# Performance work log

Measured on AMD Instinct MI355X. Metric: run time of the kernel, lower is better.

The kernel has to match this reference:

```python
import jax, jax.numpy as jnp
import numpy as np


def setup_inputs() -> dict:
    key = jax.random.key(0)
    k1, k2, k3, k4 = jax.random.split(key, 4)
    B, S, D, R = 32, 512, 1024, 256
    batch = jax.random.normal(k1, (B, S, D), dtype=jnp.float32)
    # params initialized uniform(-0.05, 0.05) in the original
    proj_L = jax.random.uniform(k2, (D, R), minval=-0.05, maxval=0.05, dtype=jnp.float32)
    proj_R = jax.random.uniform(k3, (R, D), minval=-0.05, maxval=0.05, dtype=jnp.float32)
    bias = jax.random.uniform(k4, (1,), minval=-0.05, maxval=0.05, dtype=jnp.float32)
    return {"batch": batch, "proj_L": proj_L, "proj_R": proj_R, "bias": bias}


def reference(batch, proj_L, proj_R, bias):
    # logits[b,i,j] = batch[b,i] @ (L @ R) @ batch[b,j] + bias
    # Computed as (batch @ L) @ (batch @ R^T)^T -- two batched GEMMs,
    # avoiding the O(B*S^2*D) expanded intermediate of the original.
    # Dropout is identity in eval mode.
    left = jnp.einsum('bsd,dr->bsr', batch, proj_L)   # [B,S,R]
    right = jnp.einsum('rd,btd->brt', proj_R, batch)  # [B,R,S]
    logits = jnp.einsum('bsr,brt->bst', left, right) + bias[0]
    return logits
```

## Files before the change

kernel.cpp:

```cpp
#include <hip/hip_runtime.h>
#include <hip/hip_bf16.h>
#include <stdint.h>

typedef __attribute__((ext_vector_type(8))) __bf16 bf16x8;
typedef __attribute__((ext_vector_type(4))) float f32x4;

static constexpr int Bb = 32, Ss = 512, Dd = 1024, Rr = 256;

__device__ __forceinline__ void gload_lds16(const void* g, void* l) {
  __builtin_amdgcn_global_load_lds(
      (const __attribute__((address_space(1))) void*)g,
      (__attribute__((address_space(3))) void*)l, 16, 0, 0);
}

__global__ __launch_bounds__(256) void prep_kernel(
    const float* __restrict__ L, const float* __restrict__ R,
    __bf16* __restrict__ Bt) {
  int i = blockIdx.x * 256 + threadIdx.x;
  int n = i >> 10;
  int d = i & (Dd - 1);
  float v = (n < Rr) ? L[d * Rr + n] : R[(size_t)(n - Rr) * Dd + d];
  Bt[i] = (__bf16)v;
}

__global__ __launch_bounds__(512, 2) void proj_gemm(
    const float* __restrict__ batch,
    const __bf16* __restrict__ Bt,
    __bf16* __restrict__ outL,
    __bf16* __restrict__ outR) {
  const int s = (blockIdx.x & 7) * 32 + (blockIdx.x >> 3);
  const int mt = s >> 1;
  const int nt = s & 1;
  const int m0 = mt * 128, n0 = nt * 256;

  __shared__ __align__(16) char smem[49152];

  const int t = threadIdx.x;
  const int lane = t & 63;
  const int wave = t >> 6;
  const int wr = wave >> 2, wc = wave & 3;

  f32x4 acc[4][4] = {};
  f32x4 areg0, areg1;

  const int arow = t >> 2, ag = t & 3;
  const int ags = ag ^ ((arow >> 1) & 3);

  auto issueA = [&](int k0) {
    const float* src = batch + (size_t)(m0 + arow) * Dd + k0 + ag * 8;
    areg0 = *(const f32x4*)src;
    areg1 = *(const f32x4*)(src + 4);
  };
  auto writeA = [&](int buf) {
    bf16x8 v;
    v[0] = (__bf16)areg0[0]; v[1] = (__bf16)areg0[1];
    v[2] = (__bf16)areg0[2]; v[3] = (__bf16)areg0[3];
    v[4] = (__bf16)areg1[0]; v[5] = (__bf16)areg1[1];
    v[6] = (__bf16)areg1[2]; v[7] = (__bf16)areg1[3];
    *(bf16x8*)(smem + buf * 8192 + (arow * 4 + ags) * 16) = v;
  };
  auto stageB = [&](int buf, int k0) {
#pragma unroll
    for (int p = 0; p < 2; ++p) {
      int e = p * 512 + t;
      int row = e >> 2, g = e & 3;
      int gs = g ^ ((row >> 1) & 3);
      gload_lds16(Bt + (size_t)(n0 + row) * Dd + k0 + gs * 8,
                  smem + 16384 + buf * 16384 + e * 16);
    }
  };
  auto compute = [&](int buf) {
    const char* Ab = smem + buf * 8192;
    const char* Bb = smem + 16384 + buf * 16384;
    bf16x8 a[4], b[4];
    const int g = lane >> 4;
#pragma unroll
    for (int m = 0; m < 4; ++m) {
      int row = wr * 64 + m * 16 + (lane & 15);
      a[m] = *(const bf16x8*)(Ab + (row * 4 + (g ^ ((row >> 1) & 3))) * 16);
    }
#pragma unroll
    for (int n = 0; n < 4; ++n) {
      int row = wc * 64 + n * 16 + (lane & 15);
      b[n] = *(const bf16x8*)(Bb + (row * 4 + (g ^ ((row >> 1) & 3))) * 16);
    }
#pragma unroll
    for (int m = 0; m < 4; ++m)
#pragma unroll
      for (int n = 0; n < 4; ++n)
        acc[m][n] = __builtin_amdgcn_mfma_f32_16x16x32_bf16(a[m], b[n],
                                                            acc[m][n], 0, 0, 0);
  };

  issueA(0);
  stageB(0, 0);
  writeA(0);
  int cur = 0;
  for (int it = 0; it < 32; ++it) {
    if (it < 31) {
      issueA(it * 32 + 32);
      stageB(cur ^ 1, it * 32 + 32);
      asm volatile("s_waitcnt vmcnt(4)" ::: "memory");
    } else {
      asm volatile("s_waitcnt vmcnt(0)" ::: "memory");
    }
    __builtin_amdgcn_s_barrier();
    compute(cur);
    if (it < 31) writeA(cur ^ 1);
    asm volatile("s_waitcnt lgkmcnt(0)" ::: "memory");
    __builtin_amdgcn_s_barrier();
    cur ^= 1;
  }

  __bf16* out = nt ? outR : outL;
  const int col = lane & 15, rgrp = lane >> 4;
#pragma unroll
  for (int m = 0; m < 4; ++m) {
    int r0 = m0 + wr * 64 + m * 16 + rgrp * 4;
#pragma unroll
    for (int n = 0; n < 4; ++n) {
      int c = wc * 64 + n * 16 + col;
#pragma unroll
      for (int i = 0; i < 4; ++i)
        out[(size_t)(r0 + i) * Rr + c] = (__bf16)acc[m][n][i];
    }
  }
}

__global__ __launch_bounds__(256, 4) void score_gemm(
    const __bf16* __restrict__ left,
    const __bf16* __restrict__ right,
    const float* __restrict__ biasp,
    float* __restrict__ out) {
  const int nt = blockIdx.x;
  const int mt = blockIdx.y;
  const int bz = blockIdx.z;
  const __bf16* A = left + (size_t)bz * Ss * Rr;
  const __bf16* B = right + (size_t)bz * Ss * Rr;
  float* O = out + (size_t)bz * Ss * Ss;
  const int m0 = mt * 64, n0 = nt * 128;

  __shared__ __align__(16) char smem[24576];

  const int t = threadIdx.x;
  const int lane = t & 63;
  const int wave = t >> 6;
  const int wr = wave >> 1, wc = wave & 1;

  f32x4 acc[2][4] = {};

  for (int it = 0; it < 4; ++it) {
    const int k0 = it * 64;
    __syncthreads();
#pragma unroll
    for (int q = 0; q < 2; ++q) {
      int e = q * 256 + t;
      int row = e >> 3, g = e & 7;
      int gsrc = g ^ (row & 7);
      gload_lds16(A + (size_t)(m0 + row) * Rr + k0 + gsrc * 8, smem + e * 16);
    }
#pragma unroll
    for (int q = 0; q < 4; ++q) {
      int e = q * 256 + t;
      int row = e >> 3, g = e & 7;
      int gsrc = g ^ (row & 7);
      gload_lds16(B + (size_t)(n0 + row) * Rr + k0 + gsrc * 8,
                  smem + 8192 + e * 16);
    }
    __syncthreads();

#pragma unroll
    for (int kk = 0; kk < 2; ++kk) {
      bf16x8 a[2], b[4];
#pragma unroll
      for (int m = 0; m < 2; ++m) {
        int row = wr * 32 + m * 16 + (lane & 15);
        int g = kk * 4 + (lane >> 4);
        a[m] = *(const bf16x8*)(smem + (row * 8 + (g ^ (row & 7))) * 16);
      }
#pragma unroll
      for (int n = 0; n < 4; ++n) {
        int row = wc * 64 + n * 16 + (lane & 15);
        int g = kk * 4 + (lane >> 4);
        b[n] = *(const bf16x8*)(smem + 8192 +
                                (row * 8 + (g ^ (row & 7))) * 16);
      }
#pragma unroll
      for (int m = 0; m < 2; ++m)
#pragma unroll
        for (int n = 0; n < 4; ++n)
          acc[m][n] = __builtin_amdgcn_mfma_f32_16x16x32_bf16(a[m], b[n],
                                                              acc[m][n], 0, 0, 0);
    }
  }

  const float bias = *biasp;
  const int col = lane & 15, rgrp = lane >> 4;
#pragma unroll
  for (int m = 0; m < 2; ++m) {
    int r0 = m0 + wr * 32 + m * 16 + rgrp * 4;
#pragma unroll
    for (int n = 0; n < 4; ++n) {
      int c = n0 + wc * 64 + n * 16 + col;
#pragma unroll
      for (int i = 0; i < 4; ++i)
        O[(size_t)(r0 + i) * Ss + c] = acc[m][n][i] + bias;
    }
  }
}

extern "C" void kernel_launch(void* const* d_in, const int* in_sizes, int n_in,
                              void* d_out, int out_size, void* d_ws,
                              size_t ws_size, hipStream_t stream) {
  const float* batch = (const float*)d_in[0];
  const float* projL = (const float*)d_in[1];
  const float* projR = (const float*)d_in[2];
  const float* bias = (const float*)d_in[3];
  float* out = (float*)d_out;

  char* ws = (char*)d_ws;
  __bf16* left = (__bf16*)(ws);
  __bf16* right = (__bf16*)(ws + 8388608);
  __bf16* Btc = (__bf16*)(ws + 16777216);

  prep_kernel<<<dim3(2048), dim3(256), 0, stream>>>(projL, projR, Btc);
  proj_gemm<<<dim3(256), dim3(512), 0, stream>>>(batch, Btc, left, right);
  score_gemm<<<dim3(4, 8, 32), dim3(256), 0, stream>>>(left, right, bias, out);
}
```

Baseline: 54.28 us.

## Reshape projection GEMM tile to 256x128 with K=64 stages

The projection GEMM tile changes from 128x256 to 256x128, and each pipeline step now covers 64 elements of K instead of 32. That halves the number of barrier-separated iterations. The LDS layout moves to an 8-group XOR swizzle, and the loop is restructured: the next A and B tiles are issued before compute, and the wait and barrier come after the LDS write. The cost is a larger LDS footprint (96KB), which likely limits residency to one block per CU. Each batch row is also now read by four N-tiles instead of two, so the kernel leans more on L2 reuse.

```diff
diff --git a/kernel.cpp b/kernel.cpp
--- a/kernel.cpp
+++ b/kernel.cpp
@@ -28,98 +28,115 @@
     const __bf16* __restrict__ Bt,
     __bf16* __restrict__ outL,
     __bf16* __restrict__ outR) {
-  const int s = (blockIdx.x & 7) * 32 + (blockIdx.x >> 3);
-  const int mt = s >> 1;
-  const int nt = s & 1;
-  const int m0 = mt * 128, n0 = nt * 256;
-
-  __shared__ __align__(16) char smem[49152];
+  const int s = ((blockIdx.x & 7) << 5) + (blockIdx.x >> 3);
+  const int mt = s >> 2;
+  const int nt = s & 3;
+  const int m0 = mt * 256, n0 = nt * 128;
+
+  __shared__ __align__(16) char smem[98304];
 
   const int t = threadIdx.x;
   const int lane = t & 63;
   const int wave = t >> 6;
-  const int wr = wave >> 2, wc = wave & 3;
+  const int wr = wave >> 1, wc = wave & 1;
 
   f32x4 acc[4][4] = {};
-  f32x4 areg0, areg1;
-
-  const int arow = t >> 2, ag = t & 3;
-  const int ags = ag ^ ((arow >> 1) & 3);
+  f32x4 areg[8];
 
   auto issueA = [&](int k0) {
-    const float* src = batch + (size_t)(m0 + arow) * Dd + k0 + ag * 8;
-    areg0 = *(const f32x4*)src;
-    areg1 = *(const f32x4*)(src + 4);
+#pragma unroll
+    for (int q = 0; q < 4; ++q) {
+      int e = q * 512 + t;
+      int row = e >> 3, g = e & 7;
+      const float* src = batch + (size_t)(m0 + row) * Dd + k0 + g * 8;
+      areg[2 * q] = *(const f32x4*)src;
+      areg[2 * q + 1] = *(const f32x4*)(src + 4);
+    }
   };
   auto writeA = [&](int buf) {
-    bf16x8 v;
-    v[0] = (__bf16)areg0[0]; v[1] = (__bf16)areg0[1];
-    v[2] = (__bf16)areg0[2]; v[3] = (__bf16)areg0[3];
-    v[4] = (__bf16)areg1[0]; v[5] = (__bf16)areg1[1];
-    v[6] = (__bf16)areg1[2]; v[7] = (__bf16)areg1[3];
-    *(bf16x8*)(smem + buf * 8192 + (arow * 4 + ags) * 16) = v;
+    char* Ab = smem + buf * 32768;
+#pragma unroll
+    for (int q = 0; q < 4; ++q) {
+      int e = q * 512 + t;
+      int row = e >> 3, g = e & 7;
+      int gs = g ^ (row & 7);
+      f32x4 f0 = areg[2 * q], f1 = areg[2 * q + 1];
+      bf16x8 v;
+      v[0] = (__bf16)f0[0]; v[1] = (__bf16)f0[1];
+      v[2] = (__bf16)f0[2]; v[3] = (__bf16)f0[3];
+      v[4] = (__bf16)f1[0]; v[5] = (__bf16)f1[1];
+      v[6] = (__bf16)f1[2]; v[7] = (__bf16)f1[3];
+      *(bf16x8*)(Ab + (row * 8 + gs) * 16) = v;
+    }
   };
   auto stageB = [&](int buf, int k0) {
+    char* Bbuf = smem + 65536 + buf * 16384;
 #pragma unroll
     for (int p = 0; p < 2; ++p) {
       int e = p * 512 + t;
-      int row = e >> 2, g = e & 3;
-      int gs = g ^ ((row >> 1) & 3);
+      int row = e >> 3, g = e & 7;
+      int gs = g ^ (row & 7);
       gload_lds16(Bt + (size_t)(n0 + row) * Dd + k0 + gs * 8,
-                  smem + 16384 + buf * 16384 + e * 16);
+                  Bbuf + e * 16);
     }
   };
   auto compute = [&](int buf) {
-    const char* Ab = smem + buf * 8192;
-    const char* Bb = smem + 16384 + buf * 16384;
-    bf16x8 a[4], b[4];
-    const int g = lane >> 4;
-#pragma unroll
-    for (int m = 0; m < 4; ++m) {
-      int row = wr * 64 + m * 16 + (lane & 15);
-      a[m] = *(const bf16x8*)(Ab + (row * 4 + (g ^ ((row >> 1) & 3))) * 16);
-    }
-#pragma unroll
-    for (int n = 0; n < 4; ++n) {
-      int row = wc * 64 + n * 16 + (lane & 15);
-      b[n] = *(const bf16x8*)(Bb + (row * 4 + (g ^ ((row >> 1) & 3))) * 16);
-    }
-#pragma unroll
-    for (int m = 0; m < 4; ++m)
-#pragma unroll
-      for (int n = 0; n < 4; ++n)
-        acc[m][n] = __builtin_amdgcn_mfma_f32_16x16x32_bf16(a[m], b[n],
-                                                            acc[m][n], 0, 0, 0);
+    const char* Ab = smem + buf * 32768;
+    const char* Bbuf = smem + 65536 + buf * 16384;
+#pragma unroll
+    for (int kk = 0; kk < 2; ++kk) {
+      const int g = kk * 4 + (lane >> 4);
+      bf16x8 a[4], b[4];
+#pragma unroll
+      for (int m = 0; m < 4; ++m) {
+        int row = wr * 64 + m * 16 + (lane & 15);
+        a[m] = *(const bf16x8*)(Ab + (row * 8 + (g ^ (row & 7))) * 16);
+      }
+#pragma unroll
+      for (int n = 0; n < 4; ++n) {
+        int row = wc * 64 + n * 16 + (lane & 15);
+        b[n] = *(const bf16x8*)(Bbuf + (row * 8 + (g ^ (row & 7))) * 16);
+      }
+#pragma unroll
+      for (int m = 0; m < 4; ++m)
+#pragma unroll
+        for (int n = 0; n < 4; ++n)
+          acc[m][n] = __builtin_amdgcn_mfma_f32_16x16x32_bf16(a[m], b[n],
+                                                              acc[m][n], 0, 0, 0);
+    }
   };
 
   issueA(0);
   stageB(0, 0);
   writeA(0);
-  int cur = 0;
-  for (int it = 0; it < 32; ++it) {
-    if (it < 31) {
-      issueA(it * 32 + 32);
-      stageB(cur ^ 1, it * 32 + 32);
-      asm volatile("s_waitcnt vmcnt(4)" ::: "memory");
-    } else {
+  asm volatile("s_waitcnt vmcnt(0)" ::: "memory");
+  asm volatile("s_waitcnt lgkmcnt(0)" ::: "memory");
+  __builtin_amdgcn_s_barrier();
+
+  for (int tt = 0; tt < 16; ++tt) {
+    const int buf = tt & 1;
+    if (tt < 15) {
+      issueA(tt * 64 + 64);
+      stageB(buf ^ 1, tt * 64 + 64);
+    }
+    compute(buf);
+    if (tt < 15) {
+      writeA(buf ^ 1);
       asm volatile("s_waitcnt vmcnt(0)" ::: "memory");
-    }
-    __builtin_amdgcn_s_barrier();
-    compute(cur);
-    if (it < 31) writeA(cur ^ 1);
-    asm volatile("s_waitcnt lgkmcnt(0)" ::: "memory");
-    __builtin_amdgcn_s_barrier();
-    cur ^= 1;
-  }
-
-  __bf16* out = nt ? outR : outL;
+      asm volatile("s_waitcnt lgkmcnt(0)" ::: "memory");
+      __builtin_amdgcn_s_barrier();
+    }
+  }
+
+  __bf16* out = (n0 < Rr) ? outL : outR;
+  const int cb = n0 & (Rr - 1);
   const int col = lane & 15, rgrp = lane >> 4;
 #pragma unroll
   for (int m = 0; m < 4; ++m) {
     int r0 = m0 + wr * 64 + m * 16 + rgrp * 4;
 #pragma unroll
     for (int n = 0; n < 4; ++n) {
-      int c = wc * 64 + n * 16 + col;
+      int c = cb + wc * 64 + n * 16 + col;
 #pragma unroll
       for (int i = 0; i < 4; ++i)
         out[(size_t)(r0 + i) * Rr + c] = (__bf16)acc[m][n][i];
```

New measurement: 51.73 us. 1.05x faster.
